# Performance work log

Measured on AMD Instinct MI355X. Metric: run time of the kernel, lower is better.

The kernel has to match this reference:

```python
import jax, jax.numpy as jnp
import numpy as np

D_MODEL = 192
D_STATE = 16
D_CONV = 3
EXPAND = 2
D_INNER = EXPAND * D_MODEL
DT_RANK = (D_MODEL + 15) // 16  # ceil(d_model/16) = 12


def setup_inputs() -> dict:
    key = jax.random.key(0)
    ks = jax.random.split(key, 8)
    B, H, W = 4, 32, 32
    sc = lambda n: 1.0 / np.sqrt(n)
    x = jax.random.normal(ks[0], (B, H, W, D_MODEL), jnp.float32)
    W_in = jax.random.normal(ks[1], (D_MODEL, 2 * D_INNER), jnp.float32) * sc(D_MODEL)
    conv_w = jax.random.normal(ks[2], (D_INNER, 1, D_CONV, D_CONV), jnp.float32) * sc(D_CONV * D_CONV)
    conv_b = jnp.zeros((D_INNER,), jnp.float32)
    W_x = jax.random.normal(ks[3], (D_INNER, DT_RANK + 2 * D_STATE), jnp.float32) * sc(D_INNER)
    W_dt = jax.random.normal(ks[4], (DT_RANK, D_INNER), jnp.float32) * sc(DT_RANK)
    b_dt = jnp.zeros((D_INNER,), jnp.float32)
    A_log = jnp.log(jnp.tile(jnp.arange(1, D_STATE + 1, dtype=jnp.float32), (D_INNER, 1)))
    D_param = jnp.ones((D_INNER,), jnp.float32)
    W_out = jax.random.normal(ks[5], (D_INNER, D_MODEL), jnp.float32) * sc(D_INNER)
    gamma = jnp.ones((D_INNER,), jnp.float32)
    beta = jnp.zeros((D_INNER,), jnp.float32)
    return {"x": x, "W_in": W_in, "conv_w": conv_w, "conv_b": conv_b,
            "W_x": W_x, "W_dt": W_dt, "b_dt": b_dt, "A_log": A_log,
            "D_param": D_param, "W_out": W_out, "gamma": gamma, "beta": beta}


def _ssm_scan(u, W_x, W_dt, b_dt, A_log, D_param):
    # u: (B, L, D_inner). Log-cumsum closed-form linear SSM scan.
    x_dbl = u @ W_x                                   # (B,L,dt_rank+2N)
    dt = x_dbl[..., :DT_RANK]
    B_mat = x_dbl[..., DT_RANK:DT_RANK + D_STATE]     # (B,L,N)
    C_mat = x_dbl[..., DT_RANK + D_STATE:]            # (B,L,N)
    dt = jax.nn.softplus(dt @ W_dt + b_dt)            # (B,L,D)
    A = -jnp.exp(A_log)                               # (D,N)
    log_dA = jnp.einsum('bld,dn->bldn', dt, A)        # (B,L,D,N)
    dB_u = jnp.einsum('bld,bln->bldn', dt, B_mat) * u[..., None]
    log_decay = jnp.cumsum(log_dA, axis=1)
    decay = jnp.exp(log_decay)
    h = decay * jnp.cumsum(dB_u / (decay + 1e-12), axis=1)
    y = jnp.einsum('bldn,bln->bld', h, C_mat)
    return y + u * D_param


def reference(x, W_in, conv_w, conv_b, W_x, W_dt, b_dt, A_log, D_param, W_out, gamma, beta):
    B, H, W, C = x.shape
    xz = x @ W_in                                     # (B,H,W,2*D_inner)
    x_val, z = xz[..., :D_INNER], xz[..., D_INNER:]
    # depthwise 3x3 conv in NCHW
    xc = jnp.transpose(x_val, (0, 3, 1, 2))
    xc = jax.lax.conv_general_dilated(
        xc, conv_w, window_strides=(1, 1), padding='SAME',
        feature_group_count=D_INNER,
        dimension_numbers=('NCHW', 'OIHW', 'NCHW'))
    xc = xc + conv_b[None, :, None, None]
    xc = jax.nn.silu(xc)
    xv = jnp.transpose(xc, (0, 2, 3, 1))              # (B,H,W,D_inner)

    scan = lambda u: _ssm_scan(u, W_x, W_dt, b_dt, A_log, D_param)
    s1 = xv.reshape(B, H * W, D_INNER)                # row-major
    s2 = s1[:, ::-1]
    s3 = jnp.transpose(xv, (0, 2, 1, 3)).reshape(B, W * H, D_INNER)  # column-major
    s4 = s3[:, ::-1]
    y1 = scan(s1)
    y2 = scan(s2)[:, ::-1]
    y3 = scan(s3)
    y4 = scan(s4)[:, ::-1]
    # map column-major scans back to row-major order
    y3 = jnp.transpose(y3.reshape(B, W, H, D_INNER), (0, 2, 1, 3)).reshape(B, H * W, D_INNER)
    y4 = jnp.transpose(y4.reshape(B, W, H, D_INNER), (0, 2, 1, 3)).reshape(B, H * W, D_INNER)
    y = y1 + y2 + y3 + y4

    # LayerNorm over last dim (eps=1e-5)
    mu = jnp.mean(y, axis=-1, keepdims=True)
    var = jnp.mean(jnp.square(y - mu), axis=-1, keepdims=True)
    y = (y - mu) * jax.lax.rsqrt(var + 1e-5) * gamma + beta

    y = y.reshape(B, H, W, D_INNER) * jax.nn.silu(z)
    return y @ W_out
```

## Files before the change

kernel.cpp:

```cpp
#include <hip/hip_runtime.h>
#include <hip/hip_fp16.h>

#define DMODEL 192
#define DINNER 384
#define NPOS   4096
#define SEQL   1024
#define DSTATE 16
#define DTRANK 12

__device__ __forceinline__ float silu_f(float v) { return v * (1.f / (1.f + __expf(-v))); }

__device__ __forceinline__ int scan_pos(int dir, int l) {
    int s = (dir & 1) ? (SEQL - 1 - l) : l;
    return (dir & 2) ? (((s & 31) << 5) | (s >> 5)) : s;
}

__global__ void k1_inproj(const float* __restrict__ x, const float* __restrict__ W_in,
                          float* __restrict__ x_val, float* __restrict__ gz) {
    const int t = threadIdx.x;
    const int bi = blockIdx.x;
    const int colg = bi % 3;
    const int pos0 = (bi / 3) << 3;
    const int col = colg * 256 + t;

    const float* xr = x + pos0 * DMODEL;

    float acc[8] = {0,0,0,0,0,0,0,0};
    for (int c = 0; c < DMODEL; c += 4) {
        float w0 = W_in[(c + 0) * 768 + col];
        float w1 = W_in[(c + 1) * 768 + col];
        float w2 = W_in[(c + 2) * 768 + col];
        float w3 = W_in[(c + 3) * 768 + col];
#pragma unroll
        for (int g = 0; g < 8; ++g) {
            const float4 xv = *(const float4*)&xr[g * DMODEL + c];
            acc[g] += xv.x * w0 + xv.y * w1 + xv.z * w2 + xv.w * w3;
        }
    }
    if (col < DINNER) {
#pragma unroll
        for (int g = 0; g < 8; ++g) x_val[(pos0 + g) * DINNER + col] = acc[g];
    } else {
#pragma unroll
        for (int g = 0; g < 8; ++g) gz[(pos0 + g) * DINNER + (col - DINNER)] = silu_f(acc[g]);
    }
}

__global__ void k2_conv_dt(const float* __restrict__ x_val,
                           const float* __restrict__ conv_w, const float* __restrict__ conv_b,
                           const float* __restrict__ W_x, const float* __restrict__ W_dt,
                           const float* __restrict__ b_dt, const float* __restrict__ Dp,
                           __half* __restrict__ u_out, float* __restrict__ xd_out,
                           float* __restrict__ dt32, float* __restrict__ y_acc) {
    __shared__ float us[DINNER];
    __shared__ float part[8 * 44];
    __shared__ float xdl[44];
    const int t = threadIdx.x;
    const int pos = blockIdx.x;
    const int b = pos >> 10, hw = pos & 1023, h = hw >> 5, w = hw & 31;

    float acc = conv_b[t];
#pragma unroll
    for (int i = 0; i < 3; ++i) {
        int hh = h + i - 1;
        if (hh < 0 || hh > 31) continue;
#pragma unroll
        for (int j = 0; j < 3; ++j) {
            int ww = w + j - 1;
            if (ww < 0 || ww > 31) continue;
            acc += x_val[((b * 32 + hh) * 32 + ww) * DINNER + t] * conv_w[t * 9 + i * 3 + j];
        }
    }
    float uv = silu_f(acc);
    us[t] = uv;
    u_out[pos * DINNER + t] = __float2half(uv);
    __syncthreads();

    if (t < 352) {
        int o = t % 44, p = t / 44;
        float s = 0.f;
        int j0 = p * 48;
        for (int j = j0; j < j0 + 48; ++j) s += us[j] * W_x[j * 44 + o];
        part[p * 44 + o] = s;
    }
    __syncthreads();
    if (t < 44) {
        float s = 0.f;
#pragma unroll
        for (int p = 0; p < 8; ++p) s += part[p * 44 + t];
        xd_out[pos * 48 + t] = s;
        xdl[t] = s;
    }
    __syncthreads();

    float raw = b_dt[t];
#pragma unroll
    for (int r = 0; r < DTRANK; ++r) raw += xdl[r] * W_dt[r * DINNER + t];
    dt32[pos * DINNER + t] = fmaxf(raw, 0.f) + log1pf(__expf(-fabsf(raw)));

    y_acc[pos * DINNER + t] = 4.f * Dp[t] * uv;
}

__device__ __forceinline__ void k3_load(const float* __restrict__ dtb,
                                        const float* __restrict__ xb,
                                        const __half* __restrict__ ub,
                                        int dir, int l0, int d, int n,
                                        float* dtv, float* Bv, float* Cv, float* uv, int* pk) {
#pragma unroll
    for (int k = 0; k < 8; ++k) {
        int pos = scan_pos(dir, l0 + k);
        pk[k]  = pos;
        dtv[k] = dtb[pos * DINNER + d];
        Bv[k]  = xb[pos * 48 + DTRANK + n];
        Cv[k]  = xb[pos * 48 + DTRANK + DSTATE + n];
        uv[k]  = __half2float(ub[pos * DINNER + d]);
    }
}

__device__ __forceinline__ bool k3_compute(float A, float& cum, float& S,
                                           const float* dtv, const float* Bv,
                                           const float* Cv, const float* uv, const int* pk,
                                           float* __restrict__ yb, int d, int n) {
    float decay[8];
#pragma unroll
    for (int k = 0; k < 8; ++k) { cum += dtv[k] * A; decay[k] = __expf(cum); }
    float rc[8];
#pragma unroll
    for (int k = 0; k < 8; ++k) rc[k] = __builtin_amdgcn_rcpf(decay[k] + 1e-12f);
    float c[8];
#pragma unroll
    for (int k = 0; k < 8; ++k) {
        S += (dtv[k] * Bv[k] * uv[k]) * rc[k];
        c[k] = decay[k] * S * Cv[k];
    }
#pragma unroll
    for (int off = 1; off <= 8; off <<= 1) {
#pragma unroll
        for (int k = 0; k < 8; ++k) c[k] += __shfl_xor(c[k], off);
    }
    if (n == 0) {
#pragma unroll
        for (int k = 0; k < 8; ++k) atomicAdd(&yb[pk[k] * DINNER + d], c[k]);
    }
    return __ballot(cum > -110.f) != 0ull;
}

__global__ void __launch_bounds__(256, 1)
k3_early(const __half* __restrict__ u, const float* __restrict__ xd,
         const float* __restrict__ dt32, const float* __restrict__ A_log,
         float* __restrict__ y_acc) {
    const int t = threadIdx.x;
    const int n = t & 15, dl = t >> 4;
    const int bi = blockIdx.x;
    const int chunk = bi % 24;
    const int b = (bi / 24) % 4;
    const int dir = bi / 96;
    const int d = chunk * 16 + dl;

    const float A = -__expf(A_log[d * DSTATE + n]);

    const __half* ub  = u    + b * SEQL * DINNER;
    const float* xb   = xd   + b * SEQL * 48;
    const float* dtb  = dt32 + b * SEQL * DINNER;
    float* yb = y_acc + b * SEQL * DINNER;

    float dtvA[8], BvA[8], CvA[8], uvA[8]; int pkA[8];
    float dtvB[8], BvB[8], CvB[8], uvB[8]; int pkB[8];

    float cum = 0.f, S = 0.f;
    k3_load(dtb, xb, ub, dir, 0, d, n, dtvA, BvA, CvA, uvA, pkA);
    for (int l0 = 0; l0 < SEQL; l0 += 16) {
        k3_load(dtb, xb, ub, dir, l0 + 8, d, n, dtvB, BvB, CvB, uvB, pkB);
        if (!k3_compute(A, cum, S, dtvA, BvA, CvA, uvA, pkA, yb, d, n)) break;
        int ln = (l0 + 16 < SEQL) ? (l0 + 16) : (l0 + 8);
        k3_load(dtb, xb, ub, dir, ln, d, n, dtvA, BvA, CvA, uvA, pkA);
        if (!k3_compute(A, cum, S, dtvB, BvB, CvB, uvB, pkB, yb, d, n)) break;
    }
}

__global__ void k4_out(const float* __restrict__ y_acc, const float* __restrict__ gz,
                       const float* __restrict__ gamma, const float* __restrict__ beta,
                       const float* __restrict__ W_out, float* __restrict__ out) {
    __shared__ float g_s[8 * DINNER];
    __shared__ float red[12];
    const int t = threadIdx.x;
    const int half = t / 192, tc = t % 192;
    const int lane = t & 63, wv = t >> 6;
    const int pos0 = blockIdx.x << 3;

    const float g0c = gamma[tc], g1c = gamma[tc + 192];
    const float b0c = beta[tc],  b1c = beta[tc + 192];

    for (int it = 0; it < 4; ++it) {
        int p = it * 2 + half;
        int pos = pos0 + p;
        float y0 = y_acc[pos * DINNER + tc];
        float y1 = y_acc[pos * DINNER + tc + 192];

        float s = y0 + y1;
#pragma unroll
        for (int off = 32; off > 0; off >>= 1) s += __shfl_xor(s, off);
        if (lane == 0) red[wv] = s;
        __syncthreads();
        float mu = (red[half * 3] + red[half * 3 + 1] + red[half * 3 + 2]) * (1.f / 384.f);

        float d0 = y0 - mu, d1 = y1 - mu;
        float sq = d0 * d0 + d1 * d1;
#pragma unroll
        for (int off = 32; off > 0; off >>= 1) sq += __shfl_xor(sq, off);
        if (lane == 0) red[6 + wv] = sq;
        __syncthreads();
        float var = (red[6 + half * 3] + red[6 + half * 3 + 1] + red[6 + half * 3 + 2]) * (1.f / 384.f);
        float inv = rsqrtf(var + 1e-5f);

        g_s[p * DINNER + tc]       = (d0 * inv * g0c + b0c) * gz[pos * DINNER + tc];
        g_s[p * DINNER + tc + 192] = (d1 * inv * g1c + b1c) * gz[pos * DINNER + tc + 192];
    }
    __syncthreads();

    float acc[4] = {0.f, 0.f, 0.f, 0.f};
    const int pbase = half * 4;
    for (int dd = 0; dd < DINNER; dd += 4) {
        float w0 = W_out[(dd + 0) * DMODEL + tc];
        float w1 = W_out[(dd + 1) * DMODEL + tc];
        float w2 = W_out[(dd + 2) * DMODEL + tc];
        float w3 = W_out[(dd + 3) * DMODEL + tc];
#pragma unroll
        for (int i = 0; i < 4; ++i) {
            const float4 g = *(const float4*)&g_s[(pbase + i) * DINNER + dd];
            acc[i] += g.x * w0 + g.y * w1 + g.z * w2 + g.w * w3;
        }
    }
#pragma unroll
    for (int i = 0; i < 4; ++i) out[(pos0 + pbase + i) * DMODEL + tc] = acc[i];
}

extern "C" void kernel_launch(void* const* d_in, const int* in_sizes, int n_in,
                              void* d_out, int out_size, void* d_ws, size_t ws_size,
                              hipStream_t stream) {
    (void)in_sizes; (void)n_in; (void)out_size; (void)ws_size;
    const float* x      = (const float*)d_in[0];
    const float* W_in   = (const float*)d_in[1];
    const float* conv_w = (const float*)d_in[2];
    const float* conv_b = (const float*)d_in[3];
    const float* W_x    = (const float*)d_in[4];
    const float* W_dt   = (const float*)d_in[5];
    const float* b_dt   = (const float*)d_in[6];
    const float* A_log  = (const float*)d_in[7];
    const float* Dp     = (const float*)d_in[8];
    const float* W_out  = (const float*)d_in[9];
    const float* gamma  = (const float*)d_in[10];
    const float* beta   = (const float*)d_in[11];

    char* base = (char*)d_ws;
    float*  x_val = (float*)base;
    __half* u     = (__half*)(base + 6291456);
    float*  xd    = (float*)(base + 9437184);
    float*  dt32  = (float*)(base + 10223616);
    float*  gz    = (float*)(base + 16515072);
    float*  y_acc = (float*)(base + 22806528);

    hipLaunchKernelGGL(k1_inproj, dim3(NPOS / 8 * 3), dim3(256), 0, stream, x, W_in, x_val, gz);
    hipLaunchKernelGGL(k2_conv_dt, dim3(NPOS), dim3(384), 0, stream,
                       x_val, conv_w, conv_b, W_x, W_dt, b_dt, Dp, u, xd, dt32, y_acc);
    hipLaunchKernelGGL(k3_early, dim3(384), dim3(256), 0, stream,
                       u, xd, dt32, A_log, y_acc);
    hipLaunchKernelGGL(k4_out, dim3(NPOS / 8), dim3(384), 0, stream,
                       y_acc, gz, gamma, beta, W_out, (float*)d_out);
}
```

Measured before the change: 212.6 us.

## Stage scan inputs through LDS with async global-to-LDS loads and interleaved B/C

The scan kernel now loads dt, B/C and u tiles of 32 steps into double-buffered shared memory with global_load_lds, issued by different waves, instead of having each thread do scattered per-step global loads into registers. k2 writes B and C interleaved so a B/C pair is contiguous for the tile copy. Early-exit is coordinated block-wide through a shared alive flag plus a barrier per tile. This targets latency-bound, uncoalesced loads in the sequential scan, but adds a __syncthreads per tile and relies on the async LDS copy landing before the barrier.

Measured after the change: 212.1 us. About the same (-0.3%).

```diff
diff --git a/kernel.cpp b/kernel.cpp
--- a/kernel.cpp
+++ b/kernel.cpp
@@ -7,6 +7,7 @@
 #define SEQL   1024
 #define DSTATE 16
 #define DTRANK 12
+#define TILE   32
 
 __device__ __forceinline__ float silu_f(float v) { return v * (1.f / (1.f + __expf(-v))); }
 
@@ -88,7 +89,11 @@
         float s = 0.f;
 #pragma unroll
         for (int p = 0; p < 8; ++p) s += part[p * 44 + t];
-        xd_out[pos * 48 + t] = s;
+        int o;
+        if (t < DTRANK)               o = t;
+        else if (t < DTRANK + DSTATE) o = DTRANK + 2 * (t - DTRANK);
+        else                          o = DTRANK + 1 + 2 * (t - DTRANK - DSTATE);
+        xd_out[pos * 48 + o] = s;
         xdl[t] = s;
     }
     __syncthreads();
@@ -101,26 +106,52 @@
     y_acc[pos * DINNER + t] = 4.f * Dp[t] * uv;
 }
 
-__device__ __forceinline__ void k3_load(const float* __restrict__ dtb,
-                                        const float* __restrict__ xb,
-                                        const __half* __restrict__ ub,
-                                        int dir, int l0, int d, int n,
-                                        float* dtv, float* Bv, float* Cv, float* uv, int* pk) {
+__device__ __forceinline__ void gll16(const void* g, void* l) {
+    __builtin_amdgcn_global_load_lds(
+        (const __attribute__((address_space(1))) void*)g,
+        (__attribute__((address_space(3))) void*)l, 16, 0, 0);
+}
+
+__device__ __forceinline__ void k3_stage(int l0, int dir, int d0, int wv, int lane,
+                                         const float* __restrict__ dtb,
+                                         const float* __restrict__ xb,
+                                         const __half* __restrict__ ub,
+                                         float* dt_d, float* bc_d, __half* u_d) {
+    if (wv == 0) {
+#pragma unroll
+        for (int s = 0; s < 2; ++s) {
+            int j = s * 16 + (lane >> 2);
+            int pos = scan_pos(dir, l0 + j);
+            gll16(dtb + pos * DINNER + d0 + (lane & 3) * 4, dt_d + s * 16 * 16);
+        }
+    } else if (wv == 3) {
+        int pos = scan_pos(dir, l0 + (lane >> 1));
+        gll16((const char*)ub + (size_t)(pos * DINNER + d0) * 2 + (lane & 1) * 16, u_d);
+    } else {
+        int jb0 = (wv - 1) * 16;
+#pragma unroll
+        for (int s = 0; s < 2; ++s) {
+            int jb = jb0 + s * 8;
+            int pos = scan_pos(dir, l0 + jb + (lane >> 3));
+            gll16(xb + pos * 48 + DTRANK + (lane & 7) * 4, bc_d + jb * 32);
+        }
+    }
+}
+
+__device__ __forceinline__ bool k3_chunk(float A, float& cum, float& S,
+                                         const float* __restrict__ dt_s,
+                                         const float* __restrict__ bc_s,
+                                         const __half* __restrict__ u_s,
+                                         int jb, int l0, int dir, int dl, int n,
+                                         float* __restrict__ yb, int d) {
+    float dtv[8], Bv[8], Cv[8], uv[8];
 #pragma unroll
     for (int k = 0; k < 8; ++k) {
-        int pos = scan_pos(dir, l0 + k);
-        pk[k]  = pos;
-        dtv[k] = dtb[pos * DINNER + d];
-        Bv[k]  = xb[pos * 48 + DTRANK + n];
-        Cv[k]  = xb[pos * 48 + DTRANK + DSTATE + n];
-        uv[k]  = __half2float(ub[pos * DINNER + d]);
-    }
-}
-
-__device__ __forceinline__ bool k3_compute(float A, float& cum, float& S,
-                                           const float* dtv, const float* Bv,
-                                           const float* Cv, const float* uv, const int* pk,
-                                           float* __restrict__ yb, int d, int n) {
+        dtv[k] = dt_s[(jb + k) * 16 + dl];
+        Bv[k]  = bc_s[(jb + k) * 32 + 2 * n];
+        Cv[k]  = bc_s[(jb + k) * 32 + 2 * n + 1];
+        uv[k]  = __half2float(u_s[(jb + k) * 16 + dl]);
+    }
     float decay[8];
 #pragma unroll
     for (int k = 0; k < 8; ++k) { cum += dtv[k] * A; decay[k] = __expf(cum); }
@@ -140,22 +171,31 @@
     }
     if (n == 0) {
 #pragma unroll
-        for (int k = 0; k < 8; ++k) atomicAdd(&yb[pk[k] * DINNER + d], c[k]);
+        for (int k = 0; k < 8; ++k) {
+            int pos = scan_pos(dir, l0 + jb + k);
+            atomicAdd(&yb[pos * DINNER + d], c[k]);
+        }
     }
     return __ballot(cum > -110.f) != 0ull;
 }
 
 __global__ void __launch_bounds__(256, 1)
-k3_early(const __half* __restrict__ u, const float* __restrict__ xd,
-         const float* __restrict__ dt32, const float* __restrict__ A_log,
-         float* __restrict__ y_acc) {
+k3_scan(const __half* __restrict__ u, const float* __restrict__ xd,
+        const float* __restrict__ dt32, const float* __restrict__ A_log,
+        float* __restrict__ y_acc) {
+    __shared__ float  dt_s[2][TILE * 16];
+    __shared__ float  BC_s[2][TILE * 32];
+    __shared__ __half u_s [2][TILE * 16];
+    __shared__ int    alive_w[2][4];
+
     const int t = threadIdx.x;
+    const int lane = t & 63, wv = t >> 6;
     const int n = t & 15, dl = t >> 4;
     const int bi = blockIdx.x;
     const int chunk = bi % 24;
     const int b = (bi / 24) % 4;
     const int dir = bi / 96;
-    const int d = chunk * 16 + dl;
+    const int d0 = chunk * 16, d = d0 + dl;
 
     const float A = -__expf(A_log[d * DSTATE + n]);
 
@@ -164,17 +204,29 @@
     const float* dtb  = dt32 + b * SEQL * DINNER;
     float* yb = y_acc + b * SEQL * DINNER;
 
-    float dtvA[8], BvA[8], CvA[8], uvA[8]; int pkA[8];
-    float dtvB[8], BvB[8], CvB[8], uvB[8]; int pkB[8];
+    k3_stage(0, dir, d0, wv, lane, dtb, xb, ub, dt_s[0], BC_s[0], u_s[0]);
+    __syncthreads();
 
     float cum = 0.f, S = 0.f;
-    k3_load(dtb, xb, ub, dir, 0, d, n, dtvA, BvA, CvA, uvA, pkA);
-    for (int l0 = 0; l0 < SEQL; l0 += 16) {
-        k3_load(dtb, xb, ub, dir, l0 + 8, d, n, dtvB, BvB, CvB, uvB, pkB);
-        if (!k3_compute(A, cum, S, dtvA, BvA, CvA, uvA, pkA, yb, d, n)) break;
-        int ln = (l0 + 16 < SEQL) ? (l0 + 16) : (l0 + 8);
-        k3_load(dtb, xb, ub, dir, ln, d, n, dtvA, BvA, CvA, uvA, pkA);
-        if (!k3_compute(A, cum, S, dtvB, BvB, CvB, uvB, pkB, yb, d, n)) break;
+    bool alive = true;
+    int buf = 0, par = 0;
+    for (int l0 = 0; l0 < SEQL; l0 += TILE) {
+        const int ln = (l0 + TILE < SEQL) ? (l0 + TILE) : l0;
+        k3_stage(ln, dir, d0, wv, lane, dtb, xb, ub,
+                 dt_s[buf ^ 1], BC_s[buf ^ 1], u_s[buf ^ 1]);
+        if (alive) {
+#pragma unroll
+            for (int jb = 0; jb < TILE; jb += 8) {
+                alive = k3_chunk(A, cum, S, dt_s[buf], BC_s[buf], u_s[buf],
+                                 jb, l0, dir, dl, n, yb, d);
+                if (!alive) break;
+            }
+        }
+        if (lane == 0) alive_w[par][wv] = alive ? 1 : 0;
+        __syncthreads();
+        const int any = alive_w[par][0] | alive_w[par][1] | alive_w[par][2] | alive_w[par][3];
+        buf ^= 1; par ^= 1;
+        if (!any) return;
     }
 }
 
@@ -263,7 +315,7 @@
     hipLaunchKernelGGL(k1_inproj, dim3(NPOS / 8 * 3), dim3(256), 0, stream, x, W_in, x_val, gz);
     hipLaunchKernelGGL(k2_conv_dt, dim3(NPOS), dim3(384), 0, stream,
                        x_val, conv_w, conv_b, W_x, W_dt, b_dt, Dp, u, xd, dt32, y_acc);
-    hipLaunchKernelGGL(k3_early, dim3(384), dim3(256), 0, stream,
+    hipLaunchKernelGGL(k3_scan, dim3(384), dim3(256), 0, stream,
                        u, xd, dt32, A_log, y_acc);
     hipLaunchKernelGGL(k4_out, dim3(NPOS / 8), dim3(384), 0, stream,
                        y_acc, gz, gamma, beta, W_out, (float*)d_out);
```
